# Kernel tuning notes

Hardware: AMD Instinct MI355X
Metric: run time of the kernel (lower is better)

The kernel has to match this reference:

```python
import jax, jax.numpy as jnp
import numpy as np

TWO_PI = 2.0 * np.pi


def setup_inputs() -> dict:
    key = jax.random.key(0)
    k1, k2 = jax.random.split(key)
    # positions: [batch=1, N=1024 patches, D=2 spatial axes], values in [0,1)
    positions = jax.random.uniform(k1, (1, 1024, 2), dtype=jnp.float32)
    # learned generator params: [D=2, L=4 layers, G=128 generators, g=8, g=8]
    gen_params = jax.random.uniform(k2, (2, 4, 128, 8, 8), dtype=jnp.float32) * TWO_PI
    return {"positions": positions, "gen_params": gen_params}


def reference(positions, gen_params):
    # phase_type == 'learned' branch
    # upper triangle (strictly above diagonal) shifted by -0.5; the shift
    # cancels in the skew-symmetrization, matching the torch code exactly.
    upper = jnp.triu(gen_params, k=1) - 0.5
    bases = upper - jnp.swapaxes(upper, -1, -2)  # skew-symmetric [D,L,G,g,g]
    # position-weighted sum over spatial axes D: [1,N,L,G,g,g]
    gen_pos = jnp.einsum('bnd,dlgij->bnlgij', positions, bases)
    # prepend zero generator for the cls token -> identity rotation
    cls = jnp.zeros_like(gen_pos[:, :1])
    gen_pos = jnp.concatenate([cls, gen_pos], axis=1)  # [1,N+1,L,G,g,g]
    # batched matrix exponential of tiny 8x8 skew-symmetric matrices
    shape = gen_pos.shape
    g = shape[-1]
    rot = jax.vmap(jax.scipy.linalg.expm)(
        gen_pos.astype(jnp.float32).reshape(-1, g, g)
    ).reshape(shape)
    return rot
```

## Files before the change

kernel.cpp:

```cpp
#include <hip/hip_runtime.h>
#include <cstdint>

constexpr int LG   = 512;
constexpr int NPOS = 1025;
constexpr int NMAT = NPOS * LG;
constexpr int GEN_ELEMS = 2 * LG * 64;

__host__ __device__ constexpr int UI(int i, int j) { return i*7 - (i*(i-1))/2 + (j - i - 1); }
__host__ __device__ constexpr int SI(int i, int j) { return i*8 - (i*(i-1))/2 + (j - i); }

#define YSsym(a,b)  Ys [ (a)<=(b) ? SI(a,b) : SI(b,a) ]
#define Y2sym(a,b)  Y2s[ (a)<=(b) ? SI(a,b) : SI(b,a) ]
#define EEsym(a,b)  Zs [ (a)<=(b) ? SI(a,b) : SI(b,a) ]
#define OOsym(a,b)  Y2s[ (a)<=(b) ? SI(a,b) : SI(b,a) ]
#define XV(i,k) ( (i)<(k) ? U[UI(i,k)] : -U[UI(k,i)] )

__device__ __forceinline__ void sq64(float (&D)[64], const float (&S)[64]) {
    #pragma unroll
    for (int i = 0; i < 8; ++i)
        #pragma unroll
        for (int j = 0; j < 8; ++j) {
            float acc = S[i*8+0] * S[0*8+j];
            #pragma unroll
            for (int k = 1; k < 8; ++k)
                acc = fmaf(S[i*8+k], S[k*8+j], acc);
            D[i*8+j] = acc;
        }
}

__global__ __launch_bounds__(256)
void liere_tr_kernel(const float* __restrict__ g, float* __restrict__ gT) {
    int t = blockIdx.x * 256 + threadIdx.x;
    if (t >= GEN_ELEMS) return;
    int d  = t >> 15;
    int lg = (t >> 6) & 511;
    int e  = t & 63;
    gT[(size_t)e * 1024 + lg * 2 + d] = g[t];
}

template<bool TR>
__global__ __launch_bounds__(256)
void liere_expm_kernel(const float* __restrict__ pos,
                       const float* __restrict__ gen,
                       const float* __restrict__ genT,
                       float* __restrict__ out)
{
    const int bid = blockIdx.x, tid = threadIdx.x;
    const int n   = bid >> 1;
    const int lg  = ((bid & 1) << 8) | tid;

    float P[64];

    if (n == 0) {
        #pragma unroll
        for (int i = 0; i < 8; ++i)
            #pragma unroll
            for (int j = 0; j < 8; ++j)
                P[i*8+j] = (i == j) ? 1.f : 0.f;
    } else {
        const float p0 = pos[(n-1)*2 + 0];
        const float p1 = pos[(n-1)*2 + 1];

        float U[28];
        if (TR) {
            #pragma unroll
            for (int i = 0; i < 8; ++i)
                #pragma unroll
                for (int j = i+1; j < 8; ++j) {
                    const int e = i*8 + j;
                    float2 v = *reinterpret_cast<const float2*>(
                                   genT + (size_t)e * 1024 + lg * 2);
                    U[UI(i,j)] = fmaf(p0, v.x, p1 * v.y);
                }
        } else {
            const float* g0 = gen + (size_t)lg * 64;
            const float* g1 = g0 + (size_t)LG * 64;
            #pragma unroll
            for (int i = 0; i < 8; ++i)
                #pragma unroll
                for (int j = i+1; j < 8; ++j) {
                    const int e = i*8 + j;
                    U[UI(i,j)] = fmaf(p0, g0[e], p1 * g1[e]);
                }
        }

        float Ys[36];
        #pragma unroll
        for (int i = 0; i < 8; ++i)
            #pragma unroll
            for (int j = i; j < 8; ++j) {
                float acc = 0.f;
                #pragma unroll
                for (int k = 0; k < 8; ++k) {
                    if (k == i || k == j) continue;
                    acc = fmaf(XV(i,k), XV(k,j), acc);
                }
                Ys[SI(i,j)] = acc;
            }

        float Y2s[36];
        #pragma unroll
        for (int i = 0; i < 8; ++i)
            #pragma unroll
            for (int j = i; j < 8; ++j) {
                float acc = YSsym(i,0) * YSsym(0,j);
                #pragma unroll
                for (int k = 1; k < 8; ++k)
                    acc = fmaf(YSsym(i,k), YSsym(k,j), acc);
                Y2s[SI(i,j)] = acc;
            }

        float trY = 0.f;
        #pragma unroll
        for (int i = 0; i < 8; ++i) trY += Ys[SI(i,i)];
        float dYY=0.f, oYY=0.f, dY3=0.f, oY3=0.f, d44=0.f, o44=0.f;
        #pragma unroll
        for (int i = 0; i < 8; ++i)
            #pragma unroll
            for (int j = i; j < 8; ++j) {
                float y = Ys[SI(i,j)], y2 = Y2s[SI(i,j)];
                if (i == j) { dYY=fmaf(y,y,dYY); dY3=fmaf(y,y2,dY3); d44=fmaf(y2,y2,d44); }
                else        { oYY=fmaf(y,y,oYY); oY3=fmaf(y,y2,oY3); o44=fmaf(y2,y2,o44); }
            }
        const float sYY = fmaf(2.f, oYY, dYY);
        const float sY3 = fmaf(2.f, oY3, dY3);
        const float s44 = fmaf(2.f, o44, d44);

        float yb = 0.f;
        #pragma unroll
        for (int i = 0; i < 8; ++i) {
            float rs = fabsf(Y2sym(i,0));
            #pragma unroll
            for (int j = 1; j < 8; ++j) rs += fabsf(Y2sym(i,j));
            yb = fmaxf(yb, rs);
        }
        float q4 = fmaxf(fminf(yb, 0.5f * s44), 1e-30f);
        #pragma unroll
        for (int off = 32; off >= 1; off >>= 1)
            q4 = fmaxf(q4, __shfl_xor(q4, off, 64));
        int r = (int)ceilf(0.25f * __log2f(q4) - 3.0f);
        if (r < 0) r = 0;
        if (r > 5) r = 5;

        const double R2 = (double)__uint_as_float((uint32_t)(127 - 2*r) << 23);
        const double R4 = R2 * R2;
        const double P1 = -0.5 * (double)trY * R2;
        const double P2 =  0.5 * (double)sYY * R4;
        const double P3 = -0.5 * (double)sY3 * R4 * R2;
        const double P4 =  0.5 * (double)s44 * R4 * R4;
        const double E1 = P1;
        const double E2 = 0.5 * (E1*P1 - P2);
        const double E3 = (1.0/3.0) * (E2*P1 - E1*P2 + P3);
        const double E4 = 0.25 * (E3*P1 - E2*P2 + E1*P3 - P4);

        float cf[8];
        {
            double c[16] = {
                1.0, 0.5, 0.041666666666666664, 0.001388888888888889,
                2.48015873015873e-5, 2.755731922398589e-7, 2.08767569878681e-9,
                1.1470745597729725e-11, 4.779477332387385e-14,
                1.5619206968586225e-16, 4.110317623312165e-19,
                8.896791392450574e-22, 1.6117375710961184e-24,
                2.4795962632247976e-27, 3.279889237069838e-30,
                3.7699876288159054e-33
            };
            #pragma unroll
            for (int m = 15; m >= 4; --m) {
                double t = c[m];
                c[m-1] = fma(-E1, t, c[m-1]);
                c[m-2] = fma(-E2, t, c[m-2]);
                c[m-3] = fma(-E3, t, c[m-3]);
                c[m-4] = fma(-E4, t, c[m-4]);
            }
            cf[0] = (float)c[0];
            cf[2] = (float)(c[1] * R2);
            cf[4] = (float)(c[2] * R4);
            cf[6] = (float)(c[3] * R4 * R2);
        }
        {
            double c[15] = {
                1.0, 0.16666666666666666, 0.008333333333333333,
                1.984126984126984e-4, 2.7557319223985893e-6,
                2.505210838544172e-8, 1.6059043836821613e-10,
                7.647163731819816e-13, 2.8114572543455206e-15,
                8.22063524662433e-18, 1.9572941063391263e-20,
                3.868170170630684e-23, 6.446950284384474e-26,
                9.183689863795546e-29, 1.1309962886447716e-31
            };
            #pragma unroll
            for (int m = 14; m >= 4; --m) {
                double t = c[m];
                c[m-1] = fma(-E1, t, c[m-1]);
                c[m-2] = fma(-E2, t, c[m-2]);
                c[m-3] = fma(-E3, t, c[m-3]);
                c[m-4] = fma(-E4, t, c[m-4]);
            }
            const double W1 = (double)__uint_as_float((uint32_t)(127 - r) << 23);
            cf[1] = (float)(c[0] * W1);
            cf[3] = (float)(c[1] * W1 * R2);
            cf[5] = (float)(c[2] * W1 * R4);
            cf[7] = (float)(c[3] * W1 * R4 * R2);
        }

        float Zs[36];
        #pragma unroll
        for (int i = 0; i < 8; ++i)
            #pragma unroll
            for (int j = i; j < 8; ++j) {
                float acc = YSsym(i,0) * Y2sym(0,j);
                #pragma unroll
                for (int k = 1; k < 8; ++k)
                    acc = fmaf(YSsym(i,k), Y2sym(k,j), acc);
                Zs[SI(i,j)] = acc;
            }

        #pragma unroll
        for (int k = 0; k < 36; ++k) {
            float y = Ys[k], y2 = Y2s[k], z = Zs[k];
            Zs[k]  = fmaf(cf[6], z, fmaf(cf[4], y2, cf[2]*y));
            Y2s[k] = fmaf(cf[7], z, fmaf(cf[5], y2, cf[3]*y));
        }
        #pragma unroll
        for (int i = 0; i < 8; ++i) {
            Zs[SI(i,i)]  += cf[0];
            Y2s[SI(i,i)] += cf[1];
        }

        #pragma unroll
        for (int i = 0; i < 8; ++i)
            #pragma unroll
            for (int j = 0; j < 8; ++j) {
                float acc = EEsym(i,j);
                #pragma unroll
                for (int k = 0; k < 8; ++k) {
                    if (k == i) continue;
                    acc = fmaf(XV(i,k), OOsym(k,j), acc);
                }
                P[i*8+j] = acc;
            }

        {
            float Q[64];
            int pairs = r >> 1;
            while (pairs--) { sq64(Q, P); sq64(P, Q); }
            if (r & 1) {
                sq64(Q, P);
                #pragma unroll
                for (int t = 0; t < 64; ++t) P[t] = Q[t];
            }
        }
    }

    __shared__ float4 ls[256 * 8];
    float4* o4base = reinterpret_cast<float4*>(out) + (size_t)bid * 4096;
    #pragma unroll
    for (int rr = 0; rr < 2; ++rr) {
        if (rr) __syncthreads();
        #pragma unroll
        for (int j = 0; j < 8; ++j) {
            const int jj = rr*8 + j;
            ls[tid*8 + ((j + tid) & 7)] =
                make_float4(P[4*jj+0], P[4*jj+1], P[4*jj+2], P[4*jj+3]);
        }
        __syncthreads();
        #pragma unroll
        for (int k = 0; k < 8; ++k) {
            const int u = k*256 + tid;
            const int o = u >> 3, cidx = u & 7;
            o4base[o*16 + cidx + 8*rr] = ls[o*8 + ((cidx + o) & 7)];
        }
    }
}

extern "C" void kernel_launch(void* const* d_in, const int* in_sizes, int n_in,
                              void* d_out, int out_size, void* d_ws, size_t ws_size,
                              hipStream_t stream) {
    const float* pos = (const float*)d_in[0];
    const float* gen = (const float*)d_in[1];
    float* out = (float*)d_out;

    const int block = 256;
    const int grid  = NMAT / block;

    if (ws_size >= (size_t)GEN_ELEMS * sizeof(float)) {
        float* genT = (float*)d_ws;
        liere_tr_kernel<<<GEN_ELEMS / 256, 256, 0, stream>>>(gen, genT);
        liere_expm_kernel<true><<<grid, block, 0, stream>>>(pos, gen, genT, out);
    } else {
        liere_expm_kernel<false><<<grid, block, 0, stream>>>(pos, gen, nullptr, out);
    }
}
```

Before: 51.40 us.

## Use packed float2 FMA for 8x8 matrix products instead of symmetric scalar storage

Rewrites the per-thread 8x8 matrix arithmetic on two-wide float vectors so the compiler can emit packed FP32 FMA instructions. The upper-triangle-only storage of symmetric products (Y, Y^2, Z) is replaced by full dense matrices. This roughly doubles the multiply-adds for the symmetric products but halves the instruction count through packing. It also removes the conditional index selects and fuses the Z computation with the polynomial combination row by row. The risks are higher register pressure from full 64-element matrices and more raw FLOPs.

```diff
diff --git a/kernel.cpp b/kernel.cpp
--- a/kernel.cpp
+++ b/kernel.cpp
@@ -6,25 +6,39 @@
 constexpr int NMAT = NPOS * LG;
 constexpr int GEN_ELEMS = 2 * LG * 64;
 
+typedef float v2 __attribute__((ext_vector_type(2)));
+
+__device__ __forceinline__ v2 sp(float s) { v2 r; r.x = s; r.y = s; return r; }
+__device__ __forceinline__ v2 fma2(v2 a, v2 b, v2 c) {
+#if __has_builtin(__builtin_elementwise_fma)
+    return __builtin_elementwise_fma(a, b, c);
+#else
+    v2 r; r.x = fmaf(a.x, b.x, c.x); r.y = fmaf(a.y, b.y, c.y); return r;
+#endif
+}
+__device__ __forceinline__ v2 abs2(v2 a) {
+#if __has_builtin(__builtin_elementwise_abs)
+    return __builtin_elementwise_abs(a);
+#else
+    v2 r; r.x = fabsf(a.x); r.y = fabsf(a.y); return r;
+#endif
+}
+
 __host__ __device__ constexpr int UI(int i, int j) { return i*7 - (i*(i-1))/2 + (j - i - 1); }
-__host__ __device__ constexpr int SI(int i, int j) { return i*8 - (i*(i-1))/2 + (j - i); }
-
-#define YSsym(a,b)  Ys [ (a)<=(b) ? SI(a,b) : SI(b,a) ]
-#define Y2sym(a,b)  Y2s[ (a)<=(b) ? SI(a,b) : SI(b,a) ]
-#define EEsym(a,b)  Zs [ (a)<=(b) ? SI(a,b) : SI(b,a) ]
-#define OOsym(a,b)  Y2s[ (a)<=(b) ? SI(a,b) : SI(b,a) ]
-#define XV(i,k) ( (i)<(k) ? U[UI(i,k)] : -U[UI(k,i)] )
-
-__device__ __forceinline__ void sq64(float (&D)[64], const float (&S)[64]) {
+
+#define EL(M,i,k) (M[i][(k)>>1][(k)&1])
+
+__device__ __forceinline__ void mmp(v2 (&D)[8][4], const v2 (&A)[8][4],
+                                    const v2 (&B)[8][4]) {
     #pragma unroll
     for (int i = 0; i < 8; ++i)
         #pragma unroll
-        for (int j = 0; j < 8; ++j) {
-            float acc = S[i*8+0] * S[0*8+j];
+        for (int jp = 0; jp < 4; ++jp) {
+            v2 acc = sp(EL(A,i,0)) * B[0][jp];
             #pragma unroll
             for (int k = 1; k < 8; ++k)
-                acc = fmaf(S[i*8+k], S[k*8+j], acc);
-            D[i*8+j] = acc;
+                acc = fma2(sp(EL(A,i,k)), B[k][jp], acc);
+            D[i][jp] = acc;
         }
 }
 
@@ -49,14 +63,16 @@
     const int n   = bid >> 1;
     const int lg  = ((bid & 1) << 8) | tid;
 
-    float P[64];
+    v2 P[8][4];
 
     if (n == 0) {
         #pragma unroll
         for (int i = 0; i < 8; ++i)
             #pragma unroll
-            for (int j = 0; j < 8; ++j)
-                P[i*8+j] = (i == j) ? 1.f : 0.f;
+            for (int jp = 0; jp < 4; ++jp) {
+                P[i][jp].x = (2*jp   == i) ? 1.f : 0.f;
+                P[i][jp].y = (2*jp+1 == i) ? 1.f : 0.f;
+            }
     } else {
         const float p0 = pos[(n-1)*2 + 0];
         const float p1 = pos[(n-1)*2 + 1];
@@ -84,55 +100,44 @@
                 }
         }
 
-        float Ys[36];
+        v2 Y[8][4];
+        {
+            v2 X[8][4];
+            #pragma unroll
+            for (int i = 0; i < 8; ++i)
+                #pragma unroll
+                for (int jp = 0; jp < 4; ++jp) {
+                    const int j0 = 2*jp, j1 = 2*jp+1;
+                    X[i][jp].x = (i < j0) ? U[UI(i,j0)] : (i > j0) ? -U[UI(j0,i)] : 0.f;
+                    X[i][jp].y = (i < j1) ? U[UI(i,j1)] : (i > j1) ? -U[UI(j1,i)] : 0.f;
+                }
+            mmp(Y, X, X);
+        }
+
+        v2 Y2[8][4];
+        mmp(Y2, Y, Y);
+
+        float trY = 0.f;
+        #pragma unroll
+        for (int i = 0; i < 8; ++i) trY += EL(Y,i,i);
+        v2 a2 = sp(0.f), a3 = sp(0.f), a4 = sp(0.f);
         #pragma unroll
         for (int i = 0; i < 8; ++i)
             #pragma unroll
-            for (int j = i; j < 8; ++j) {
-                float acc = 0.f;
-                #pragma unroll
-                for (int k = 0; k < 8; ++k) {
-                    if (k == i || k == j) continue;
-                    acc = fmaf(XV(i,k), XV(k,j), acc);
-                }
-                Ys[SI(i,j)] = acc;
-            }
-
-        float Y2s[36];
-        #pragma unroll
-        for (int i = 0; i < 8; ++i)
-            #pragma unroll
-            for (int j = i; j < 8; ++j) {
-                float acc = YSsym(i,0) * YSsym(0,j);
-                #pragma unroll
-                for (int k = 1; k < 8; ++k)
-                    acc = fmaf(YSsym(i,k), YSsym(k,j), acc);
-                Y2s[SI(i,j)] = acc;
-            }
-
-        float trY = 0.f;
-        #pragma unroll
-        for (int i = 0; i < 8; ++i) trY += Ys[SI(i,i)];
-        float dYY=0.f, oYY=0.f, dY3=0.f, oY3=0.f, d44=0.f, o44=0.f;
-        #pragma unroll
-        for (int i = 0; i < 8; ++i)
-            #pragma unroll
-            for (int j = i; j < 8; ++j) {
-                float y = Ys[SI(i,j)], y2 = Y2s[SI(i,j)];
-                if (i == j) { dYY=fmaf(y,y,dYY); dY3=fmaf(y,y2,dY3); d44=fmaf(y2,y2,d44); }
-                else        { oYY=fmaf(y,y,oYY); oY3=fmaf(y,y2,oY3); o44=fmaf(y2,y2,o44); }
-            }
-        const float sYY = fmaf(2.f, oYY, dYY);
-        const float sY3 = fmaf(2.f, oY3, dY3);
-        const float s44 = fmaf(2.f, o44, d44);
+            for (int jp = 0; jp < 4; ++jp) {
+                a2 = fma2(Y[i][jp],  Y[i][jp],  a2);
+                a3 = fma2(Y[i][jp],  Y2[i][jp], a3);
+                a4 = fma2(Y2[i][jp], Y2[i][jp], a4);
+            }
+        const float sYY = a2.x + a2.y;
+        const float sY3 = a3.x + a3.y;
+        const float s44 = a4.x + a4.y;
 
         float yb = 0.f;
         #pragma unroll
         for (int i = 0; i < 8; ++i) {
-            float rs = fabsf(Y2sym(i,0));
-            #pragma unroll
-            for (int j = 1; j < 8; ++j) rs += fabsf(Y2sym(i,j));
-            yb = fmaxf(yb, rs);
+            v2 s = abs2(Y2[i][0]) + abs2(Y2[i][1]) + abs2(Y2[i][2]) + abs2(Y2[i][3]);
+            yb = fmaxf(yb, s.x + s.y);
         }
         float q4 = fmaxf(fminf(yb, 0.5f * s44), 1e-30f);
         #pragma unroll
@@ -202,51 +207,52 @@
             cf[7] = (float)(c[3] * W1 * R4 * R2);
         }
 
-        float Zs[36];
+        v2 O[8][4];
+        #pragma unroll
+        for (int k = 0; k < 8; ++k) {
+            v2 Zr[4];
+            #pragma unroll
+            for (int jp = 0; jp < 4; ++jp) {
+                v2 acc = sp(EL(Y,k,0)) * Y2[0][jp];
+                #pragma unroll
+                for (int m = 1; m < 8; ++m)
+                    acc = fma2(sp(EL(Y,k,m)), Y2[m][jp], acc);
+                Zr[jp] = acc;
+            }
+            #pragma unroll
+            for (int jp = 0; jp < 4; ++jp) {
+                v2 y = Y[k][jp], y2 = Y2[k][jp], z = Zr[jp];
+                O[k][jp] = fma2(sp(cf[7]), z, fma2(sp(cf[5]), y2, sp(cf[3]) * y));
+                Y[k][jp] = fma2(sp(cf[6]), z, fma2(sp(cf[4]), y2, sp(cf[2]) * y));
+            }
+            EL(Y,k,k) += cf[0];
+            EL(O,k,k) += cf[1];
+        }
+
         #pragma unroll
         for (int i = 0; i < 8; ++i)
             #pragma unroll
-            for (int j = i; j < 8; ++j) {
-                float acc = YSsym(i,0) * Y2sym(0,j);
-                #pragma unroll
-                for (int k = 1; k < 8; ++k)
-                    acc = fmaf(YSsym(i,k), Y2sym(k,j), acc);
-                Zs[SI(i,j)] = acc;
-            }
-
-        #pragma unroll
-        for (int k = 0; k < 36; ++k) {
-            float y = Ys[k], y2 = Y2s[k], z = Zs[k];
-            Zs[k]  = fmaf(cf[6], z, fmaf(cf[4], y2, cf[2]*y));
-            Y2s[k] = fmaf(cf[7], z, fmaf(cf[5], y2, cf[3]*y));
-        }
-        #pragma unroll
-        for (int i = 0; i < 8; ++i) {
-            Zs[SI(i,i)]  += cf[0];
-            Y2s[SI(i,i)] += cf[1];
-        }
-
-        #pragma unroll
-        for (int i = 0; i < 8; ++i)
-            #pragma unroll
-            for (int j = 0; j < 8; ++j) {
-                float acc = EEsym(i,j);
+            for (int jp = 0; jp < 4; ++jp) {
+                v2 acc = Y[i][jp];
                 #pragma unroll
                 for (int k = 0; k < 8; ++k) {
                     if (k == i) continue;
-                    acc = fmaf(XV(i,k), OOsym(k,j), acc);
-                }
-                P[i*8+j] = acc;
-            }
-
-        {
-            float Q[64];
+                    const float xik = (i < k) ? U[UI(i,k)] : -U[UI(k,i)];
+                    acc = fma2(sp(xik), O[k][jp], acc);
+                }
+                P[i][jp] = acc;
+            }
+
+        {
+            v2 Q[8][4];
             int pairs = r >> 1;
-            while (pairs--) { sq64(Q, P); sq64(P, Q); }
+            while (pairs--) { mmp(Q, P, P); mmp(P, Q, Q); }
             if (r & 1) {
-                sq64(Q, P);
-                #pragma unroll
-                for (int t = 0; t < 64; ++t) P[t] = Q[t];
+                mmp(Q, P, P);
+                #pragma unroll
+                for (int i = 0; i < 8; ++i)
+                    #pragma unroll
+                    for (int jp = 0; jp < 4; ++jp) P[i][jp] = Q[i][jp];
             }
         }
     }
@@ -259,8 +265,9 @@
         #pragma unroll
         for (int j = 0; j < 8; ++j) {
             const int jj = rr*8 + j;
+            const int i = jj >> 1, h = jj & 1;
             ls[tid*8 + ((j + tid) & 7)] =
-                make_float4(P[4*jj+0], P[4*jj+1], P[4*jj+2], P[4*jj+3]);
+                make_float4(P[i][2*h].x, P[i][2*h].y, P[i][2*h+1].x, P[i][2*h+1].y);
         }
         __syncthreads();
         #pragma unroll
```

New measurement: 74.23 us. 44.4% more time.

## Pick scaling from Newton spectral-radius estimate and exploit symmetric/skew structure in assembly

Applied to the files above, without the earlier changes.

Replaces the row-sum norm bound used to choose the squaring count with a Newton solve for the largest root of the characteristic quartic, built from the trace invariants. This is meant to give a tighter estimate and so fewer squarings. The diagonal constants are folded into the coefficient combine loop. Final assembly now uses even-symmetric plus odd-skew structure, computing only the upper triangle and mirroring it as e±acc, which roughly halves the FMAs. The risk is that an underestimated radius, from a non-converged Newton iteration or from the 4-term truncation, loses accuracy.

```diff
diff --git a/kernel.cpp b/kernel.cpp
--- a/kernel.cpp
+++ b/kernel.cpp
@@ -126,32 +126,38 @@
         const float sY3 = fmaf(2.f, oY3, dY3);
         const float s44 = fmaf(2.f, o44, d44);
 
-        float yb = 0.f;
-        #pragma unroll
-        for (int i = 0; i < 8; ++i) {
-            float rs = fabsf(Y2sym(i,0));
-            #pragma unroll
-            for (int j = 1; j < 8; ++j) rs += fabsf(Y2sym(i,j));
-            yb = fmaxf(yb, rs);
-        }
-        float q4 = fmaxf(fminf(yb, 0.5f * s44), 1e-30f);
+        const double P1u = -0.5 * (double)trY;
+        const double P2u =  0.5 * (double)sYY;
+        const double P3u = -0.5 * (double)sY3;
+        const double P4u =  0.5 * (double)s44;
+        const double E1u = P1u;
+        const double E2u = 0.5 * (E1u*P1u - P2u);
+        const double E3u = (1.0/3.0) * (E2u*P1u - E1u*P2u + P3u);
+        const double E4u = 0.25 * (E3u*P1u - E2u*P2u + E1u*P3u - P4u);
+
+        const float e1f = (float)E1u, e2f = (float)E2u,
+                    e3f = (float)E3u, e4f = (float)E4u;
+        float mu = fmaxf(e1f, 1e-12f);
+        #pragma unroll
+        for (int it = 0; it < 5; ++it) {
+            float f  = fmaf(fmaf(fmaf(mu - e1f, mu, e2f), mu, -e3f), mu, e4f);
+            float fp = fmaf(fmaf(fmaf(4.f, mu, -3.f*e1f), mu, 2.f*e2f), mu, -e3f);
+            mu = mu - __fdividef(f, fp);
+        }
+        mu = fmaxf(mu, 1e-12f);
         #pragma unroll
         for (int off = 32; off >= 1; off >>= 1)
-            q4 = fmaxf(q4, __shfl_xor(q4, off, 64));
-        int r = (int)ceilf(0.25f * __log2f(q4) - 3.0f);
+            mu = fmaxf(mu, __shfl_xor(mu, off, 64));
+        int r = (int)ceilf(0.5f * __log2f(mu) - 3.0f);
         if (r < 0) r = 0;
         if (r > 5) r = 5;
 
         const double R2 = (double)__uint_as_float((uint32_t)(127 - 2*r) << 23);
         const double R4 = R2 * R2;
-        const double P1 = -0.5 * (double)trY * R2;
-        const double P2 =  0.5 * (double)sYY * R4;
-        const double P3 = -0.5 * (double)sY3 * R4 * R2;
-        const double P4 =  0.5 * (double)s44 * R4 * R4;
-        const double E1 = P1;
-        const double E2 = 0.5 * (E1*P1 - P2);
-        const double E3 = (1.0/3.0) * (E2*P1 - E1*P2 + P3);
-        const double E4 = 0.25 * (E3*P1 - E2*P2 + E1*P3 - P4);
+        const double E1 = E1u * R2;
+        const double E2 = E2u * R4;
+        const double E3 = E3u * R4 * R2;
+        const double E4 = E4u * R4 * R4;
 
         float cf[8];
         {
@@ -215,29 +221,33 @@
             }
 
         #pragma unroll
-        for (int k = 0; k < 36; ++k) {
-            float y = Ys[k], y2 = Y2s[k], z = Zs[k];
-            Zs[k]  = fmaf(cf[6], z, fmaf(cf[4], y2, cf[2]*y));
-            Y2s[k] = fmaf(cf[7], z, fmaf(cf[5], y2, cf[3]*y));
-        }
+        for (int i = 0; i < 8; ++i)
+            #pragma unroll
+            for (int j = i; j < 8; ++j) {
+                const int k = SI(i,j);
+                float y = Ys[k], y2 = Y2s[k], z = Zs[k];
+                float eb = (i == j) ? fmaf(cf[2], y, cf[0]) : cf[2] * y;
+                float ob = (i == j) ? fmaf(cf[3], y, cf[1]) : cf[3] * y;
+                Zs[k]  = fmaf(cf[6], z, fmaf(cf[4], y2, eb));
+                Y2s[k] = fmaf(cf[7], z, fmaf(cf[5], y2, ob));
+            }
+
         #pragma unroll
         for (int i = 0; i < 8; ++i) {
-            Zs[SI(i,i)]  += cf[0];
-            Y2s[SI(i,i)] += cf[1];
-        }
-
-        #pragma unroll
-        for (int i = 0; i < 8; ++i)
-            #pragma unroll
-            for (int j = 0; j < 8; ++j) {
-                float acc = EEsym(i,j);
+            P[i*8+i] = EEsym(i,i);
+            #pragma unroll
+            for (int j = i+1; j < 8; ++j) {
+                float acc = 0.f;
                 #pragma unroll
                 for (int k = 0; k < 8; ++k) {
                     if (k == i) continue;
                     acc = fmaf(XV(i,k), OOsym(k,j), acc);
                 }
-                P[i*8+j] = acc;
-            }
+                float e = EEsym(i,j);
+                P[i*8+j] = e + acc;
+                P[j*8+i] = e - acc;
+            }
+        }
 
         {
             float Q[64];
```

After: 49.74 us, median of 2. -3.2%, faster.
